# Kernel optimization log

Measured on AMD Instinct MI355X. Metric: run time of the kernel, lower is better.

Reference implementation:

```python
import jax, jax.numpy as jnp
import numpy as np

DIM = 768
HEADS = 12
DIM_HEAD = 64
INNER = HEADS * DIM_HEAD  # 768
EPS = 1e-5


def setup_inputs() -> dict:
    key = jax.random.key(0)
    ks = jax.random.split(key, 5)
    x = jax.random.normal(ks[0], (4, 2048, DIM), dtype=jnp.float32)
    ln_g = jnp.ones((DIM,), dtype=jnp.float32)
    ln_b = jnp.zeros((DIM,), dtype=jnp.float32)
    s1 = 1.0 / np.sqrt(DIM)
    W_qkv = jax.random.uniform(ks[1], (DIM, 3 * INNER), dtype=jnp.float32, minval=-s1, maxval=s1)
    b_qkv = jax.random.uniform(ks[2], (3 * INNER,), dtype=jnp.float32, minval=-s1, maxval=s1)
    s2 = 1.0 / np.sqrt(INNER)
    W_out = jax.random.uniform(ks[3], (INNER, DIM), dtype=jnp.float32, minval=-s2, maxval=s2)
    b_out = jax.random.uniform(ks[4], (DIM,), dtype=jnp.float32, minval=-s2, maxval=s2)
    return {"x": x, "ln_g": ln_g, "ln_b": ln_b, "W_qkv": W_qkv, "b_qkv": b_qkv, "W_out": W_out, "b_out": b_out}


def reference(x, ln_g, ln_b, W_qkv, b_qkv, W_out, b_out):
    b, n, _ = x.shape
    # pre-norm LayerNorm
    mu = jnp.mean(x, axis=-1, keepdims=True)
    var = jnp.mean(jnp.square(x - mu), axis=-1, keepdims=True)
    xn = (x - mu) * jax.lax.rsqrt(var + EPS) * ln_g + ln_b
    qkv = xn @ W_qkv + b_qkv  # [b, n, 3*inner]
    q, k, v = jnp.split(qkv, 3, axis=-1)
    def to_heads(t):
        return t.reshape(b, n, HEADS, DIM_HEAD).transpose(0, 2, 1, 3)  # b h n d
    q, k, v = map(to_heads, (q, k, v))
    q = q * (DIM_HEAD ** -0.5)
    sim = jnp.einsum('bhid,bhjd->bhij', q, k)
    attn = jax.nn.softmax(sim, axis=-1)  # dropout is identity (p=0.0)
    out = jnp.einsum('bhij,bhjd->bhid', attn, v)
    out = out.transpose(0, 2, 1, 3).reshape(b, n, INNER)
    return out @ W_out + b_out
```

## Files before the change

### kernel.cpp

```cpp
#include <hip/hip_runtime.h>
#include <cstdint>
#include <cstddef>


#define SEQ    2048
#define NBATCH 4
#define DMODEL 768
#define NHEADS 12
#define DHEAD  64
#define MROWS  (NBATCH * SEQ)
#define NQKV   (3 * DMODEL)
#define KT     64
#define NT     (SEQ / KT)

using f32x4  = __attribute__((ext_vector_type(4))) float;
using u16x8  = __attribute__((ext_vector_type(8))) unsigned short;
using s16x8  = __attribute__((ext_vector_type(8))) short;
using u16x4  = __attribute__((ext_vector_type(4))) unsigned short;
using s16x4  = __attribute__((ext_vector_type(4))) short;

__device__ __forceinline__ unsigned short f2bf(float f) {
  union { float f; unsigned int u; } x; x.f = f;
  unsigned int r = x.u + 0x7fffu + ((x.u >> 16) & 1u);
  return (unsigned short)(r >> 16);
}

#if defined(__has_builtin)
#if __has_builtin(__builtin_amdgcn_cvt_pk_bf16_f32)
#define HAVE_PK_BF16 1
#endif
#if __has_builtin(__builtin_amdgcn_exp2f)
#define HAVE_EXP2 1
#endif
#if __has_builtin(__builtin_amdgcn_mfma_f32_16x16x16bf16_1k)
#define HAVE_MFMA_16X16X16_BF16 1
#endif
#endif

__device__ __forceinline__ unsigned int pk_bf16(float a, float b) {
#ifdef HAVE_PK_BF16
  auto v = __builtin_amdgcn_cvt_pk_bf16_f32(a, b);
  union { decltype(v) v2; unsigned int u; } c; c.v2 = v; return c.u;
#else
  return (unsigned int)f2bf(a) | ((unsigned int)f2bf(b) << 16);
#endif
}

__device__ __forceinline__ float fexp2(float x) {
#ifdef HAVE_EXP2
  return __builtin_amdgcn_exp2f(x);
#else
  return exp2f(x);
#endif
}

__device__ __forceinline__ f32x4 mfma16(u16x8 a, u16x8 b, f32x4 c) {
  return __builtin_amdgcn_mfma_f32_16x16x32_bf16((s16x8)a, (s16x8)b, c, 0, 0, 0);
}

__device__ __forceinline__ f32x4 mfma16k16(u16x4 a, u16x4 b, f32x4 c) {
#ifdef HAVE_MFMA_16X16X16_BF16
  return __builtin_amdgcn_mfma_f32_16x16x16bf16_1k((s16x4)a, (s16x4)b, c, 0, 0, 0);
#else
  f32x4 d;
  asm("v_mfma_f32_16x16x16_bf16 %0, %1, %2, %3"
      : "=v"(d) : "v"(a), "v"(b), "v"(c));
  return d;
#endif
}

__device__ __forceinline__ void gl_lds16(const void* g, void* l) {
  __builtin_amdgcn_global_load_lds(
      (const __attribute__((address_space(1))) void*)g,
      (__attribute__((address_space(3))) void*)l, 16, 0, 0);
}

__global__ __launch_bounds__(256) void lntconv_kernel(
    const float* __restrict__ x, const float* __restrict__ g,
    const float* __restrict__ bb, unsigned short* __restrict__ xn,
    const float* __restrict__ Wq, const float* __restrict__ Wo,
    unsigned short* __restrict__ Wqt, unsigned short* __restrict__ Wot) {
  __shared__ float tile[32][33];
  const int t = threadIdx.x;
  int id = blockIdx.x;
  if (id < MROWS) {
    float* red = &tile[0][0];
    const float* xr = x + (size_t)id * DMODEL;
    float v0 = xr[t], v1 = xr[t + 256], v2 = xr[t + 512];
    float s = v0 + v1 + v2;
#pragma unroll
    for (int o = 32; o; o >>= 1) s += __shfl_down(s, o);
    if ((t & 63) == 0) red[t >> 6] = s;
    __syncthreads();
    float mu = (red[0] + red[1] + red[2] + red[3]) * (1.0f / DMODEL);
    float d0 = v0 - mu, d1 = v1 - mu, d2 = v2 - mu;
    float q = d0 * d0 + d1 * d1 + d2 * d2;
#pragma unroll
    for (int o = 32; o; o >>= 1) q += __shfl_down(q, o);
    if ((t & 63) == 0) red[4 + (t >> 6)] = q;
    __syncthreads();
    float var = (red[4] + red[5] + red[6] + red[7]) * (1.0f / DMODEL);
    float rstd = rsqrtf(var + 1e-5f);
    size_t base = (size_t)id * DMODEL;
    xn[base + t]       = f2bf(d0 * rstd * g[t]       + bb[t]);
    xn[base + t + 256] = f2bf(d1 * rstd * g[t + 256] + bb[t + 256]);
    xn[base + t + 512] = f2bf(d2 * rstd * g[t + 512] + bb[t + 512]);
    return;
  }
  id -= MROWS;
  const float* W; unsigned short* Wt; int N, n0, k0;
  if (id < 1728) { W = Wq; Wt = Wqt; N = NQKV;   n0 = (id % 72) * 32; k0 = (id / 72) * 32; }
  else { id -= 1728; W = Wo; Wt = Wot; N = DMODEL; n0 = (id % 24) * 32; k0 = (id / 24) * 32; }
  const int tx = t & 31, ty = t >> 5;
#pragma unroll
  for (int r = 0; r < 4; ++r)
    tile[ty + r * 8][tx] = W[(size_t)(k0 + ty + r * 8) * N + n0 + tx];
  __syncthreads();
#pragma unroll
  for (int r = 0; r < 4; ++r)
    Wt[(size_t)(n0 + ty + r * 8) * DMODEL + k0 + tx] = f2bf(tile[tx][ty + r * 8]);
}

__global__ __launch_bounds__(256, 3) void gemm_qkv_kernel(
    const unsigned short* __restrict__ Wt, const unsigned short* __restrict__ xn,
    const float* __restrict__ bias, unsigned short* __restrict__ qb,
    unsigned short* __restrict__ kb, unsigned short* __restrict__ vt) {
  __shared__ alignas(16) unsigned short As[128 * 64];
  __shared__ alignas(16) unsigned short Bs[128 * 64];
  const int t = threadIdx.x, wid = t >> 6, l = t & 63, quad = l >> 4, ll = l & 15;
  const int bid = blockIdx.x;
  const int w = (bid & 7) * 144 + (bid >> 3);
  const bool isqk = (w < 768);
  int a0, b0;
  if (isqk) { a0 = (w % 12) * 128; b0 = (w / 12) * 128; }
  else { int w2 = w - 768; a0 = (w2 & 63) * 128; b0 = 2 * DMODEL + (w2 >> 6) * 128; }
  const unsigned short* Ap = isqk ? (Wt + (size_t)a0 * DMODEL) : (xn + (size_t)a0 * DMODEL);
  const unsigned short* Bp = isqk ? (xn + (size_t)b0 * DMODEL) : (Wt + (size_t)b0 * DMODEL);
  const int wa = (wid >> 1) * 64, wb = (wid & 1) * 64;
  const int srow = l >> 3, sblk = (l & 7) ^ srow;
  f32x4 acc[4][4] = {};
  for (int k0 = 0; k0 < DMODEL; k0 += 64) {
#pragma unroll
    for (int cc = 0; cc < 4; ++cc) {
      int call = wid * 4 + cc;
      int r = call * 8 + srow;
      gl_lds16(Ap + (size_t)r * DMODEL + k0 + sblk * 8, &As[call * 512]);
      gl_lds16(Bp + (size_t)r * DMODEL + k0 + sblk * 8, &Bs[call * 512]);
    }
    __syncthreads();
#pragma unroll
    for (int ks = 0; ks < 2; ++ks) {
      u16x8 af[4], bf[4];
#pragma unroll
      for (int i = 0; i < 4; ++i) {
        int ra = wa + i * 16 + ll, rb = wb + i * 16 + ll;
        int blk = (ks * 4 + quad) ^ (ll & 7);
        af[i] = *(const u16x8*)&As[ra * 64 + blk * 8];
        bf[i] = *(const u16x8*)&Bs[rb * 64 + blk * 8];
      }
#pragma unroll
      for (int mi = 0; mi < 4; ++mi)
#pragma unroll
        for (int ni = 0; ni < 4; ++ni)
          acc[mi][ni] = mfma16(af[mi], bf[ni], acc[mi][ni]);
    }
    __syncthreads();
  }
  if (isqk) {
    const bool isq = (a0 < DMODEL);
    unsigned short* dst = isq ? qb : kb;
    const float sc = isq ? 0.18033688f : 1.0f;
#pragma unroll
    for (int mi = 0; mi < 4; ++mi) {
      int row0 = a0 + wa + mi * 16 + quad * 4;
      float4 bv = *(const float4*)&bias[row0];
      int rr = isq ? row0 : row0 - DMODEL;
      int h = rr >> 6, d0 = rr & 63;
#pragma unroll
      for (int ni = 0; ni < 4; ++ni) {
        int seq = b0 + wb + ni * 16 + ll;
        int b = seq >> 11, i = seq & 2047;
        uint2 pk;
        pk.x = pk_bf16((acc[mi][ni][0] + bv.x) * sc, (acc[mi][ni][1] + bv.y) * sc);
        pk.y = pk_bf16((acc[mi][ni][2] + bv.z) * sc, (acc[mi][ni][3] + bv.w) * sc);
        *(uint2*)&dst[(size_t)((b * NHEADS + h) * SEQ + i) * DHEAD + d0] = pk;
      }
    }
  } else {
#pragma unroll
    for (int mi = 0; mi < 4; ++mi) {
      int gm = a0 + wa + mi * 16 + quad * 4;
      int b = gm >> 11, i0 = gm & 2047;
#pragma unroll
      for (int ni = 0; ni < 4; ++ni) {
        int gn = b0 + wb + ni * 16 + ll;
        float bv = bias[gn];
        int rem = gn - 2 * DMODEL;
        int h = rem >> 6, d = rem & 63;
        int bh = b * NHEADS + h;
        uint2 pk;
        pk.x = pk_bf16(acc[mi][ni][0] + bv, acc[mi][ni][1] + bv);
        pk.y = pk_bf16(acc[mi][ni][2] + bv, acc[mi][ni][3] + bv);
        *(uint2*)&vt[((size_t)bh * DHEAD + d) * SEQ + i0] = pk;
      }
    }
  }
}

__global__ __launch_bounds__(256, 3) void attn_kernel(
    const unsigned short* __restrict__ qbuf, const unsigned short* __restrict__ kbuf,
    const unsigned short* __restrict__ vtg, unsigned short* __restrict__ ao) {
  __shared__ alignas(16) unsigned short stage[3][2][KT * DHEAD];
  const int t = threadIdx.x, wid = t >> 6, l = t & 63, quad = l >> 4, ll = l & 15;
  const int Lid = blockIdx.y * 16 + blockIdx.x;
  const int w = (Lid & 7) * 96 + (Lid >> 3);
  const int qt = w & 15, bh = w >> 4;
  const unsigned short* qg  = qbuf + ((size_t)bh * SEQ + qt * 128) * DHEAD;
  const unsigned short* kg0 = kbuf + (size_t)bh * SEQ * DHEAD;
  const unsigned short* vt0 = vtg  + (size_t)bh * DHEAD * SEQ;
  const int srow = l >> 3;
  const int sblk = (l & 7) ^ srow;

  unsigned short* Qs = &stage[0][0][0];
#pragma unroll
  for (int cc = 0; cc < 4; ++cc) {
    int call = wid * 4 + cc;
    gl_lds16(qg + (call * 8 + srow) * 64 + sblk * 8, Qs + call * 512);
  }
  __syncthreads();
  u16x8 qf[2][2];
#pragma unroll
  for (int mi = 0; mi < 2; ++mi)
#pragma unroll
    for (int ks = 0; ks < 2; ++ks) {
      int r = wid * 32 + mi * 16 + ll;
      int blk = (ks * 4 + quad) ^ (ll & 7);
      qf[mi][ks] = *(const u16x8*)&Qs[r * 64 + blk * 8];
    }
  __syncthreads();

  auto stage_tile = [&](int buf, int kt2) {
    const unsigned short* kg = kg0 + (size_t)kt2 * KT * DHEAD;
#pragma unroll
    for (int c = 0; c < 2; ++c) {
      int call = wid * 2 + c;
      int r = call * 8 + srow;
      gl_lds16(kg + r * 64 + sblk * 8, &stage[buf][0][call * 512]);
      gl_lds16(vt0 + (size_t)r * SEQ + kt2 * KT + sblk * 8, &stage[buf][1][call * 512]);
    }
  };

  f32x4 oacc[2][4] = {};
  f32x4 osum[2] = {};
  const u16x4 onesb = {0x3f80u, 0x3f80u, 0x3f80u, 0x3f80u};

  stage_tile(0, 0);
  stage_tile(1, 1);
  int bufc = 0, bufs = 2;
  for (int kt2 = 0; kt2 < NT; ++kt2) {
    if (kt2 + 1 < NT) asm volatile("s_waitcnt vmcnt(4)" ::: "memory");
    else              asm volatile("s_waitcnt vmcnt(0)" ::: "memory");
    __builtin_amdgcn_s_barrier();
    if (kt2 + 2 < NT) stage_tile(bufs, kt2 + 2);
    const unsigned short* Ks = &stage[bufc][0][0];
    const unsigned short* Vs = &stage[bufc][1][0];

    f32x4 st[2][4] = {};
    __builtin_amdgcn_s_setprio(1);
#pragma unroll
    for (int ks = 0; ks < 2; ++ks)
#pragma unroll
      for (int ni = 0; ni < 4; ++ni) {
        int r = ni * 16 + ll;
        int blk = (ks * 4 + quad) ^ (ll & 7);
        u16x8 kf = *(const u16x8*)&Ks[r * 64 + blk * 8];
        st[0][ni] = mfma16(kf, qf[0][ks], st[0][ni]);
        st[1][ni] = mfma16(kf, qf[1][ks], st[1][ni]);
      }
    __builtin_amdgcn_s_setprio(0);

#pragma unroll
    for (int ni = 0; ni < 4; ++ni) {
      u16x4 pf[2];
#pragma unroll
      for (int mi = 0; mi < 2; ++mi) {
        float p0 = fexp2(st[mi][ni][0]);
        float p1 = fexp2(st[mi][ni][1]);
        float p2 = fexp2(st[mi][ni][2]);
        float p3 = fexp2(st[mi][ni][3]);
        union { uint2 u; u16x4 v; } cv;
        cv.u.x = pk_bf16(p0, p1);
        cv.u.y = pk_bf16(p2, p3);
        pf[mi] = cv.v;
      }
      const int voff = (((ni * 2 + (quad >> 1)) ^ (ll & 7)) << 3) + (quad & 1) * 4;
      __builtin_amdgcn_s_setprio(1);
      osum[0] = mfma16k16(pf[0], onesb, osum[0]);
      osum[1] = mfma16k16(pf[1], onesb, osum[1]);
#pragma unroll
      for (int di = 0; di < 4; ++di) {
        u16x4 vf = *(const u16x4*)&Vs[(di * 16 + ll) * 64 + voff];
        oacc[0][di] = mfma16k16(pf[0], vf, oacc[0][di]);
        oacc[1][di] = mfma16k16(pf[1], vf, oacc[1][di]);
      }
      __builtin_amdgcn_s_setprio(0);
    }
    bufc = (bufc == 2) ? 0 : bufc + 1;
    bufs = (bufs == 2) ? 0 : bufs + 1;
  }

  const int b = bh / NHEADS, h = bh - b * NHEADS;
#pragma unroll
  for (int mi = 0; mi < 2; ++mi) {
#pragma unroll
    for (int r = 0; r < 4; ++r) {
      float inv = 1.0f / osum[mi][r];
      int row = qt * 128 + wid * 32 + mi * 16 + quad * 4 + r;
      size_t base = ((size_t)(b * SEQ + row)) * DMODEL + h * DHEAD;
#pragma unroll
      for (int di = 0; di < 4; ++di)
        ao[base + di * 16 + ll] = f2bf(oacc[mi][di][r] * inv);
    }
  }
}

__global__ __launch_bounds__(256, 3) void gemm_out_kernel(
    const unsigned short* __restrict__ Wt, const unsigned short* __restrict__ ao,
    const float* __restrict__ bias, float* __restrict__ out) {
  __shared__ alignas(16) unsigned short As[64 * 64];
  __shared__ alignas(16) unsigned short Bs[128 * 64];
  const int t = threadIdx.x, wid = t >> 6, l = t & 63, quad = l >> 4, ll = l & 15;
  const int bid = blockIdx.x;
  const int w = (bid & 7) * 96 + (bid >> 3);
  const int a0 = (w % 12) * 64;
  const int b0 = (w / 12) * 128;
  const int wa = (wid >> 1) * 32, wb = (wid & 1) * 64;
  const int srow = l >> 3, sblk = (l & 7) ^ srow;
  f32x4 acc[2][4] = {};
  for (int k0 = 0; k0 < DMODEL; k0 += 64) {
#pragma unroll
    for (int cc = 0; cc < 6; ++cc) {
      int call = wid * 6 + cc;
      if (call < 8) {
        int r = call * 8 + srow;
        gl_lds16(Wt + (size_t)(a0 + r) * DMODEL + k0 + sblk * 8, &As[call * 512]);
      } else {
        int c2 = call - 8;
        int r = c2 * 8 + srow;
        gl_lds16(ao + (size_t)(b0 + r) * DMODEL + k0 + sblk * 8, &Bs[c2 * 512]);
      }
    }
    __syncthreads();
#pragma unroll
    for (int ks = 0; ks < 2; ++ks) {
      u16x8 af[2], bf[4];
#pragma unroll
      for (int i = 0; i < 2; ++i) {
        int ra = wa + i * 16 + ll;
        int blk = (ks * 4 + quad) ^ (ll & 7);
        af[i] = *(const u16x8*)&As[ra * 64 + blk * 8];
      }
#pragma unroll
      for (int i = 0; i < 4; ++i) {
        int rb = wb + i * 16 + ll;
        int blk = (ks * 4 + quad) ^ (ll & 7);
        bf[i] = *(const u16x8*)&Bs[rb * 64 + blk * 8];
      }
#pragma unroll
      for (int mi = 0; mi < 2; ++mi)
#pragma unroll
        for (int ni = 0; ni < 4; ++ni)
          acc[mi][ni] = mfma16(af[mi], bf[ni], acc[mi][ni]);
    }
    __syncthreads();
  }
#pragma unroll
  for (int mi = 0; mi < 2; ++mi) {
    int row0 = a0 + wa + mi * 16 + quad * 4;
    float4 bv = *(const float4*)&bias[row0];
#pragma unroll
    for (int ni = 0; ni < 4; ++ni) {
      int seq = b0 + wb + ni * 16 + ll;
      float4 o;
      o.x = acc[mi][ni][0] + bv.x;
      o.y = acc[mi][ni][1] + bv.y;
      o.z = acc[mi][ni][2] + bv.z;
      o.w = acc[mi][ni][3] + bv.w;
      *(float4*)&out[(size_t)seq * DMODEL + row0] = o;
    }
  }
}

extern "C" void kernel_launch(void* const* d_in, const int* in_sizes, int n_in,
                              void* d_out, int out_size, void* d_ws, size_t ws_size,
                              hipStream_t stream) {
  const float* x     = (const float*)d_in[0];
  const float* ln_g  = (const float*)d_in[1];
  const float* ln_b  = (const float*)d_in[2];
  const float* W_qkv = (const float*)d_in[3];
  const float* b_qkv = (const float*)d_in[4];
  const float* W_out = (const float*)d_in[5];
  const float* b_out = (const float*)d_in[6];
  float* out = (float*)d_out;

  char* ws = (char*)d_ws;
  unsigned short* xn    = (unsigned short*)(ws);
  unsigned short* wqkvt = (unsigned short*)(ws + 12582912);
  unsigned short* woutt = (unsigned short*)(ws + 16121856);
  unsigned short* qb    = (unsigned short*)(ws + 17301504);
  unsigned short* kb    = (unsigned short*)(ws + 29884416);
  unsigned short* vt    = (unsigned short*)(ws + 42467328);
  unsigned short* ao    = xn;

  lntconv_kernel<<<MROWS + 2304, 256, 0, stream>>>(x, ln_g, ln_b, xn,
                                                   W_qkv, W_out, wqkvt, woutt);
  gemm_qkv_kernel<<<1152, 256, 0, stream>>>(wqkvt, xn, b_qkv, qb, kb, vt);
  attn_kernel<<<dim3(SEQ / 128, NBATCH * NHEADS), 256, 0, stream>>>(qb, kb, vt, ao);
  gemm_out_kernel<<<768, 256, 0, stream>>>(woutt, ao, b_out, out);
}
```

Measured before the change: 219.3 us.

## Warp-per-row LayerNorm, merge QK and V GEMM tiles per block, unroll attention ring

```diff
diff --git a/kernel.cpp b/kernel.cpp
--- a/kernel.cpp
+++ b/kernel.cpp
@@ -83,31 +83,38 @@
   __shared__ float tile[32][33];
   const int t = threadIdx.x;
   int id = blockIdx.x;
-  if (id < MROWS) {
-    float* red = &tile[0][0];
-    const float* xr = x + (size_t)id * DMODEL;
-    float v0 = xr[t], v1 = xr[t + 256], v2 = xr[t + 512];
-    float s = v0 + v1 + v2;
-#pragma unroll
-    for (int o = 32; o; o >>= 1) s += __shfl_down(s, o);
-    if ((t & 63) == 0) red[t >> 6] = s;
-    __syncthreads();
-    float mu = (red[0] + red[1] + red[2] + red[3]) * (1.0f / DMODEL);
-    float d0 = v0 - mu, d1 = v1 - mu, d2 = v2 - mu;
-    float q = d0 * d0 + d1 * d1 + d2 * d2;
-#pragma unroll
-    for (int o = 32; o; o >>= 1) q += __shfl_down(q, o);
-    if ((t & 63) == 0) red[4 + (t >> 6)] = q;
-    __syncthreads();
-    float var = (red[4] + red[5] + red[6] + red[7]) * (1.0f / DMODEL);
-    float rstd = rsqrtf(var + 1e-5f);
-    size_t base = (size_t)id * DMODEL;
-    xn[base + t]       = f2bf(d0 * rstd * g[t]       + bb[t]);
-    xn[base + t + 256] = f2bf(d1 * rstd * g[t + 256] + bb[t + 256]);
-    xn[base + t + 512] = f2bf(d2 * rstd * g[t + 512] + bb[t + 512]);
+  if (id < 2048) {
+    const int wid = t >> 6, l = t & 63;
+    const int row = id * 4 + wid;
+    const float4* xr = (const float4*)(x + (size_t)row * DMODEL);
+    float4 xa = xr[l], xb2 = xr[64 + l], xc = xr[128 + l];
+    float s = (xa.x + xa.y) + (xa.z + xa.w) + (xb2.x + xb2.y) + (xb2.z + xb2.w)
+            + (xc.x + xc.y) + (xc.z + xc.w);
+    float q = xa.x * xa.x + xa.y * xa.y + xa.z * xa.z + xa.w * xa.w
+            + xb2.x * xb2.x + xb2.y * xb2.y + xb2.z * xb2.z + xb2.w * xb2.w
+            + xc.x * xc.x + xc.y * xc.y + xc.z * xc.z + xc.w * xc.w;
+#pragma unroll
+    for (int o = 32; o; o >>= 1) { s += __shfl_xor(s, o); q += __shfl_xor(q, o); }
+    const float mu = s * (1.0f / DMODEL);
+    const float var = q * (1.0f / DMODEL) - mu * mu;
+    const float rstd = rsqrtf(var + 1e-5f);
+    const float4* gp = (const float4*)g;
+    const float4* bp = (const float4*)bb;
+    uint2* dst = (uint2*)(xn + (size_t)row * DMODEL);
+#pragma unroll
+    for (int c = 0; c < 3; ++c) {
+      float4 xv = (c == 0) ? xa : (c == 1) ? xb2 : xc;
+      float4 gv = gp[c * 64 + l], bv = bp[c * 64 + l];
+      float y0 = (xv.x - mu) * rstd * gv.x + bv.x;
+      float y1 = (xv.y - mu) * rstd * gv.y + bv.y;
+      float y2 = (xv.z - mu) * rstd * gv.z + bv.z;
+      float y3 = (xv.w - mu) * rstd * gv.w + bv.w;
+      uint2 pk; pk.x = pk_bf16(y0, y1); pk.y = pk_bf16(y2, y3);
+      dst[c * 64 + l] = pk;
+    }
     return;
   }
-  id -= MROWS;
+  id -= 2048;
   const float* W; unsigned short* Wt; int N, n0, k0;
   if (id < 1728) { W = Wq; Wt = Wqt; N = NQKV;   n0 = (id % 72) * 32; k0 = (id / 72) * 32; }
   else { id -= 1728; W = Wo; Wt = Wot; N = DMODEL; n0 = (id % 24) * 32; k0 = (id / 24) * 32; }
@@ -129,44 +136,43 @@
   __shared__ alignas(16) unsigned short Bs[128 * 64];
   const int t = threadIdx.x, wid = t >> 6, l = t & 63, quad = l >> 4, ll = l & 15;
   const int bid = blockIdx.x;
-  const int w = (bid & 7) * 144 + (bid >> 3);
-  const bool isqk = (w < 768);
-  int a0, b0;
-  if (isqk) { a0 = (w % 12) * 128; b0 = (w / 12) * 128; }
-  else { int w2 = w - 768; a0 = (w2 & 63) * 128; b0 = 2 * DMODEL + (w2 >> 6) * 128; }
-  const unsigned short* Ap = isqk ? (Wt + (size_t)a0 * DMODEL) : (xn + (size_t)a0 * DMODEL);
-  const unsigned short* Bp = isqk ? (xn + (size_t)b0 * DMODEL) : (Wt + (size_t)b0 * DMODEL);
-  const int wa = (wid >> 1) * 64, wb = (wid & 1) * 64;
+  const int w = (bid & 7) * 96 + (bid >> 3);
   const int srow = l >> 3, sblk = (l & 7) ^ srow;
-  f32x4 acc[4][4] = {};
-  for (int k0 = 0; k0 < DMODEL; k0 += 64) {
-#pragma unroll
-    for (int cc = 0; cc < 4; ++cc) {
-      int call = wid * 4 + cc;
-      int r = call * 8 + srow;
-      gl_lds16(Ap + (size_t)r * DMODEL + k0 + sblk * 8, &As[call * 512]);
-      gl_lds16(Bp + (size_t)r * DMODEL + k0 + sblk * 8, &Bs[call * 512]);
-    }
-    __syncthreads();
-#pragma unroll
-    for (int ks = 0; ks < 2; ++ks) {
-      u16x8 af[4], bf[4];
-#pragma unroll
-      for (int i = 0; i < 4; ++i) {
-        int ra = wa + i * 16 + ll, rb = wb + i * 16 + ll;
-        int blk = (ks * 4 + quad) ^ (ll & 7);
-        af[i] = *(const u16x8*)&As[ra * 64 + blk * 8];
-        bf[i] = *(const u16x8*)&Bs[rb * 64 + blk * 8];
-      }
-#pragma unroll
-      for (int mi = 0; mi < 4; ++mi)
-#pragma unroll
-        for (int ni = 0; ni < 4; ++ni)
-          acc[mi][ni] = mfma16(af[mi], bf[ni], acc[mi][ni]);
-    }
-    __syncthreads();
-  }
-  if (isqk) {
+
+  {
+    const int a0 = (w % 12) * 128;
+    const int b0 = (w / 12) * 128;
+    const unsigned short* Ap = Wt + (size_t)a0 * DMODEL;
+    const unsigned short* Bp = xn + (size_t)b0 * DMODEL;
+    const int wa = (wid >> 1) * 64, wb = (wid & 1) * 64;
+    f32x4 acc[4][4] = {};
+    for (int k0 = 0; k0 < DMODEL; k0 += 64) {
+#pragma unroll
+      for (int cc = 0; cc < 4; ++cc) {
+        int call = wid * 4 + cc;
+        int r = call * 8 + srow;
+        gl_lds16(Ap + (size_t)r * DMODEL + k0 + sblk * 8, &As[call * 512]);
+        gl_lds16(Bp + (size_t)r * DMODEL + k0 + sblk * 8, &Bs[call * 512]);
+      }
+      __syncthreads();
+#pragma unroll
+      for (int ks = 0; ks < 2; ++ks) {
+        u16x8 af[4], bf[4];
+#pragma unroll
+        for (int i = 0; i < 4; ++i) {
+          int ra = wa + i * 16 + ll, rb = wb + i * 16 + ll;
+          int blk = (ks * 4 + quad) ^ (ll & 7);
+          af[i] = *(const u16x8*)&As[ra * 64 + blk * 8];
+          bf[i] = *(const u16x8*)&Bs[rb * 64 + blk * 8];
+        }
+#pragma unroll
+        for (int mi = 0; mi < 4; ++mi)
+#pragma unroll
+          for (int ni = 0; ni < 4; ++ni)
+            acc[mi][ni] = mfma16(af[mi], bf[ni], acc[mi][ni]);
+      }
+      __syncthreads();
+    }
     const bool isq = (a0 < DMODEL);
     unsigned short* dst = isq ? qb : kb;
     const float sc = isq ? 0.18033688f : 1.0f;
@@ -186,14 +192,59 @@
         *(uint2*)&dst[(size_t)((b * NHEADS + h) * SEQ + i) * DHEAD + d0] = pk;
       }
     }
-  } else {
-#pragma unroll
-    for (int mi = 0; mi < 4; ++mi) {
-      int gm = a0 + wa + mi * 16 + quad * 4;
+  }
+
+  {
+    const int m0 = (w & 127) * 64;
+    const int n0 = 2 * DMODEL + (w >> 7) * 128;
+    const unsigned short* Ap = xn + (size_t)m0 * DMODEL;
+    const unsigned short* Bp = Wt + (size_t)n0 * DMODEL;
+    const int wm = (wid >> 1) * 32, wn = (wid & 1) * 64;
+    f32x4 acc[2][4] = {};
+    for (int k0 = 0; k0 < DMODEL; k0 += 64) {
+#pragma unroll
+      for (int cc = 0; cc < 2; ++cc) {
+        int call = wid * 2 + cc;
+        int r = call * 8 + srow;
+        gl_lds16(Ap + (size_t)r * DMODEL + k0 + sblk * 8, &As[call * 512]);
+      }
+#pragma unroll
+      for (int cc = 0; cc < 4; ++cc) {
+        int call = wid * 4 + cc;
+        int r = call * 8 + srow;
+        gl_lds16(Bp + (size_t)r * DMODEL + k0 + sblk * 8, &Bs[call * 512]);
+      }
+      __syncthreads();
+#pragma unroll
+      for (int ks = 0; ks < 2; ++ks) {
+        u16x8 af[2], bf[4];
+#pragma unroll
+        for (int i = 0; i < 2; ++i) {
+          int ra = wm + i * 16 + ll;
+          int blk = (ks * 4 + quad) ^ (ll & 7);
+          af[i] = *(const u16x8*)&As[ra * 64 + blk * 8];
+        }
+#pragma unroll
+        for (int i = 0; i < 4; ++i) {
+          int rb = wn + i * 16 + ll;
+          int blk = (ks * 4 + quad) ^ (ll & 7);
+          bf[i] = *(const u16x8*)&Bs[rb * 64 + blk * 8];
+        }
+#pragma unroll
+        for (int mi = 0; mi < 2; ++mi)
+#pragma unroll
+          for (int ni = 0; ni < 4; ++ni)
+            acc[mi][ni] = mfma16(af[mi], bf[ni], acc[mi][ni]);
+      }
+      __syncthreads();
+    }
+#pragma unroll
+    for (int mi = 0; mi < 2; ++mi) {
+      int gm = m0 + wm + mi * 16 + quad * 4;
       int b = gm >> 11, i0 = gm & 2047;
 #pragma unroll
       for (int ni = 0; ni < 4; ++ni) {
-        int gn = b0 + wb + ni * 16 + ll;
+        int gn = n0 + wn + ni * 16 + ll;
         float bv = bias[gn];
         int rem = gn - 2 * DMODEL;
         int h = rem >> 6, d = rem & 63;
@@ -254,17 +305,9 @@
   f32x4 osum[2] = {};
   const u16x4 onesb = {0x3f80u, 0x3f80u, 0x3f80u, 0x3f80u};
 
-  stage_tile(0, 0);
-  stage_tile(1, 1);
-  int bufc = 0, bufs = 2;
-  for (int kt2 = 0; kt2 < NT; ++kt2) {
-    if (kt2 + 1 < NT) asm volatile("s_waitcnt vmcnt(4)" ::: "memory");
-    else              asm volatile("s_waitcnt vmcnt(0)" ::: "memory");
-    __builtin_amdgcn_s_barrier();
-    if (kt2 + 2 < NT) stage_tile(bufs, kt2 + 2);
-    const unsigned short* Ks = &stage[bufc][0][0];
-    const unsigned short* Vs = &stage[bufc][1][0];
-
+  auto do_tile = [&](int buf) {
+    const unsigned short* Ks = &stage[buf][0][0];
+    const unsigned short* Vs = &stage[buf][1][0];
     f32x4 st[2][4] = {};
     __builtin_amdgcn_s_setprio(1);
 #pragma unroll
@@ -278,7 +321,6 @@
         st[1][ni] = mfma16(kf, qf[1][ks], st[1][ni]);
       }
     __builtin_amdgcn_s_setprio(0);
-
 #pragma unroll
     for (int ni = 0; ni < 4; ++ni) {
       u16x4 pf[2];
@@ -305,9 +347,20 @@
       }
       __builtin_amdgcn_s_setprio(0);
     }
-    bufc = (bufc == 2) ? 0 : bufc + 1;
-    bufs = (bufs == 2) ? 0 : bufs + 1;
-  }
+  };
+
+#define VMW(N) asm volatile("s_waitcnt vmcnt(" #N ")" ::: "memory")
+  stage_tile(0, 0);
+  stage_tile(1, 1);
+#pragma unroll 1
+  for (int g = 0; g < 30; g += 3) {
+    VMW(4); __builtin_amdgcn_s_barrier(); stage_tile(2, g + 2); do_tile(0);
+    VMW(4); __builtin_amdgcn_s_barrier(); stage_tile(0, g + 3); do_tile(1);
+    VMW(4); __builtin_amdgcn_s_barrier(); stage_tile(1, g + 4); do_tile(2);
+  }
+  VMW(4); __builtin_amdgcn_s_barrier(); do_tile(0);
+  VMW(0); __builtin_amdgcn_s_barrier(); do_tile(1);
+#undef VMW
 
   const int b = bh / NHEADS, h = bh - b * NHEADS;
 #pragma unroll
@@ -412,9 +465,9 @@
   unsigned short* vt    = (unsigned short*)(ws + 42467328);
   unsigned short* ao    = xn;
 
-  lntconv_kernel<<<MROWS + 2304, 256, 0, stream>>>(x, ln_g, ln_b, xn,
-                                                   W_qkv, W_out, wqkvt, woutt);
-  gemm_qkv_kernel<<<1152, 256, 0, stream>>>(wqkvt, xn, b_qkv, qb, kb, vt);
+  lntconv_kernel<<<2048 + 2304, 256, 0, stream>>>(x, ln_g, ln_b, xn,
+                                                  W_qkv, W_out, wqkvt, woutt);
+  gemm_qkv_kernel<<<768, 256, 0, stream>>>(wqkvt, xn, b_qkv, qb, kb, vt);
   attn_kernel<<<dim3(SEQ / 128, NBATCH * NHEADS), 256, 0, stream>>>(qb, kb, vt, ao);
   gemm_out_kernel<<<768, 256, 0, stream>>>(woutt, ao, b_out, out);
 }
```

Measured after the change: 219.0 us. No clear change (-0.2%).
